# Performance work log

Measured on AMD Instinct MI355X. Metric: run time of the kernel, lower is better.

The kernel has to match this reference:

```python
import jax, jax.numpy as jnp
import numpy as np

EPS = 1e-7  # Keras backend epsilon


def setup_inputs() -> dict:
    key = jax.random.key(0)
    kx, ka, ke, kp = jax.random.split(key, 4)
    B, N, F, K_, C = 8, 2048, 128, 128, 128
    X = jax.random.normal(kx, (B, N, F), dtype=jnp.float32)
    Au = (jax.random.uniform(ka, (B, N, N)) < 0.05).astype(jnp.float32)
    A = jnp.maximum(Au, jnp.swapaxes(Au, -1, -2))
    W_emb = jax.random.normal(ke, (F, C), dtype=jnp.float32) * 0.1
    W_pool = jax.random.normal(kp, (F, K_), dtype=jnp.float32) * 0.1
    return {"X": X, "A": A, "W_emb": W_emb, "W_pool": W_pool}


def _diffpool(X, A, W_emb, W_pool):
    N = A.shape[-1]
    I = jnp.eye(N, dtype=A.dtype)
    A_ = A + I
    # symmetric normalization D^-1/2 (A+I) D^-1/2
    d = jax.lax.rsqrt(jnp.sum(A_, axis=-1))          # [B, N]
    fltr = A_ * d[..., :, None] * d[..., None, :]    # [B, N, N]

    Z = jnp.einsum('bnm,bmc->bnc', fltr, X @ W_emb)  # embedding GNN (no activation)
    S = jax.nn.softmax(jnp.einsum('bnm,bmk->bnk', fltr, X @ W_pool), axis=-1)  # [B, N, k]

    # link prediction loss: ||A - S S^T||_F per graph, mean over batch
    S_gram = jnp.einsum('bnk,bmk->bnm', S, S)
    LP_loss = jnp.mean(jnp.linalg.norm(A - S_gram, ord='fro', axis=(-1, -2)))

    # entropy loss on assignments
    entr = -jnp.sum(S * jnp.log(S + EPS), axis=-1)   # [B, N]
    entr_loss = jnp.mean(entr)

    X_pooled = jnp.einsum('bnk,bnc->bkc', S, Z)                  # S^T Z
    A_pooled = jnp.einsum('bnk,bnm,bml->bkl', S, A, S)           # S^T A S
    return X_pooled, A_pooled, S, LP_loss, entr_loss


def reference(X, A, W_emb, W_pool):
    return _diffpool(X, A, W_emb, W_pool)
```

## Files before the change

### kernel.cpp

```cpp
#include <hip/hip_runtime.h>
#include <math.h>

typedef __bf16 bf16x8 __attribute__((ext_vector_type(8)));
typedef float  f32x4  __attribute__((ext_vector_type(4)));
typedef unsigned short u16x4 __attribute__((ext_vector_type(4)));

#define DEVI __device__ __forceinline__

static constexpr int NB  = 8;
static constexpr int NN  = 2048;
static constexpr int NF  = 128;
static constexpr int NC2 = 256;
static constexpr int NSK = 16;

static constexpr int OUT_X0  = 0;
static constexpr int OUT_A0  = NB * 128 * 128;
static constexpr int OUT_S0  = OUT_A0 + NB * 128 * 128;
static constexpr int OUT_LP  = OUT_S0 + NB * NN * 128;
static constexpr int OUT_ENT = OUT_LP + 1;

DEVI unsigned short f2b(float f) {
  unsigned int u = __builtin_bit_cast(unsigned int, f);
  u += 0x7fffu + ((u >> 16) & 1u);
  return (unsigned short)(u >> 16);
}
DEVI float b2f(unsigned short h) {
  unsigned int u = ((unsigned int)h) << 16;
  return __builtin_bit_cast(float, u);
}
DEVI void load_lds16(const void* g, void* l) {
  __builtin_amdgcn_global_load_lds(
      (const __attribute__((address_space(1))) void*)g,
      (__attribute__((address_space(3))) void*)l, 16, 0, 0);
}
DEVI int swz(int row) { return (row >> 1) & 3; }

DEVI void stage_b128(const unsigned short* src, int ld, unsigned short* dst,
                     int k0, int tid) {
  const int wave = tid >> 6;
#pragma unroll
  for (int is = 0; is < 2; ++is) {
    const int row = is * 64 + (tid >> 2);
    const int c   = tid & 3;
    load_lds16(src + row * ld + k0 + ((c ^ swz(row)) << 3),
               dst + ((is * 256 + wave * 64) << 3));
  }
}
DEVI void stage_a64(const unsigned short* src, int ld, unsigned short* dst,
                    int k0, int tid) {
  const int wave = tid >> 6;
  const int row = tid >> 2, c = tid & 3;
  load_lds16(src + row * ld + k0 + ((c ^ swz(row)) << 3), dst + (wave << 9));
}

DEVI void gemm_core64(const unsigned short* Aop, int lda,
                      const unsigned short* Bop, int ldb, int ksteps,
                      unsigned short* lA0, unsigned short* lA1,
                      unsigned short* lB0, unsigned short* lB1,
                      int tid, f32x4 (&acc)[4][2]) {
  const int lane = tid & 63, wave = tid >> 6;
  const int l15 = lane & 15;
  const int sx = (lane >> 4) ^ ((l15 >> 1) & 3);
#pragma unroll
  for (int i = 0; i < 4; ++i) {
    acc[i][0] = (f32x4){0.f, 0.f, 0.f, 0.f};
    acc[i][1] = (f32x4){0.f, 0.f, 0.f, 0.f};
  }
  stage_a64(Aop, lda, lA0, 0, tid);
  stage_b128(Bop, ldb, lB0, 0, tid);
  __syncthreads();
  for (int kt = 0; kt < ksteps; ++kt) {
    unsigned short* curA = (kt & 1) ? lA1 : lA0;
    unsigned short* curB = (kt & 1) ? lB1 : lB0;
    if (kt + 1 < ksteps) {
      const int k0 = (kt + 1) * 32;
      stage_a64(Aop, lda, (kt & 1) ? lA0 : lA1, k0, tid);
      stage_b128(Bop, ldb, (kt & 1) ? lB0 : lB1, k0, tid);
    }
    bf16x8 af[4], bg[2];
#pragma unroll
    for (int i = 0; i < 4; ++i)
      af[i] = *(const bf16x8*)(curA + (((i * 16 + l15) * 4 + sx) << 3));
#pragma unroll
    for (int j = 0; j < 2; ++j)
      bg[j] = *(const bf16x8*)(curB + (((wave * 32 + j * 16 + l15) * 4 + sx) << 3));
#pragma unroll
    for (int i = 0; i < 4; ++i)
#pragma unroll
      for (int j = 0; j < 2; ++j)
        acc[i][j] = __builtin_amdgcn_mfma_f32_16x16x32_bf16(af[i], bg[j],
                                                            acc[i][j], 0, 0, 0);
    __syncthreads();
  }
}

DEVI void gemm_core128(const unsigned short* Aop, int lda,
                       const unsigned short* Bop, int ldb, int ksteps,
                       unsigned short* lA0, unsigned short* lA1,
                       unsigned short* lB0, unsigned short* lB1,
                       int tid, f32x4 (&acc)[4][4]) {
  const int lane = tid & 63, wave = tid >> 6;
  const int wr = wave >> 1, wc = wave & 1;
  const int l15 = lane & 15;
  const int sx = (lane >> 4) ^ ((l15 >> 1) & 3);
#pragma unroll
  for (int i = 0; i < 4; ++i)
#pragma unroll
    for (int j = 0; j < 4; ++j) acc[i][j] = (f32x4){0.f, 0.f, 0.f, 0.f};
  stage_b128(Aop, lda, lA0, 0, tid);
  stage_b128(Bop, ldb, lB0, 0, tid);
  __syncthreads();
  for (int kt = 0; kt < ksteps; ++kt) {
    unsigned short* curA = (kt & 1) ? lA1 : lA0;
    unsigned short* curB = (kt & 1) ? lB1 : lB0;
    if (kt + 1 < ksteps) {
      const int k0 = (kt + 1) * 32;
      stage_b128(Aop, lda, (kt & 1) ? lA0 : lA1, k0, tid);
      stage_b128(Bop, ldb, (kt & 1) ? lB0 : lB1, k0, tid);
    }
    bf16x8 af[4], bg[4];
#pragma unroll
    for (int i = 0; i < 4; ++i)
      af[i] = *(const bf16x8*)(curA + (((wr * 64 + i * 16 + l15) * 4 + sx) << 3));
#pragma unroll
    for (int j = 0; j < 4; ++j)
      bg[j] = *(const bf16x8*)(curB + (((wc * 64 + j * 16 + l15) * 4 + sx) << 3));
#pragma unroll
    for (int i = 0; i < 4; ++i)
#pragma unroll
      for (int j = 0; j < 4; ++j)
        acc[i][j] = __builtin_amdgcn_mfma_f32_16x16x32_bf16(af[i], bg[j],
                                                            acc[i][j], 0, 0, 0);
    __syncthreads();
  }
}

__global__ __launch_bounds__(256) void k_prep(const float* __restrict__ A,
                                              const float* __restrict__ X,
                                              const float* __restrict__ Wemb,
                                              const float* __restrict__ Wpool,
                                              unsigned short* __restrict__ AB,
                                              unsigned short* __restrict__ XB,
                                              unsigned short* __restrict__ WT,
                                              float* __restrict__ dvec,
                                              float* __restrict__ rsum) {
  const int blk = blockIdx.x, tid = threadIdx.x;
  if (blk < 4096) {
    const int row = blk * 4 + (tid >> 6);
    const int lane = tid & 63;
    const f32x4* src = (const f32x4*)(A + ((size_t)row << 11));
    u16x4* dst = (u16x4*)(AB + ((size_t)row << 11));
    float s = 0.f;
#pragma unroll
    for (int it = 0; it < 8; ++it) {
      f32x4 v = src[it * 64 + lane];
      s += v[0] + v[1] + v[2] + v[3];
      u16x4 o;
      o[0] = f2b(v[0]); o[1] = f2b(v[1]); o[2] = f2b(v[2]); o[3] = f2b(v[3]);
      dst[it * 64 + lane] = o;
    }
#pragma unroll
    for (int o2 = 32; o2; o2 >>= 1) s += __shfl_down(s, o2);
    if (lane == 0) { dvec[row] = rsqrtf(s + 1.f); rsum[row] = s; }
  } else if (blk < 4608) {
    const int i0 = (blk - 4096) * 1024 + tid;
    const f32x4* src = (const f32x4*)X;
    u16x4* dst = (u16x4*)XB;
#pragma unroll
    for (int it = 0; it < 4; ++it) {
      const int idx = i0 + it * 256;
      f32x4 v = src[idx];
      u16x4 o;
      o[0] = f2b(v[0]); o[1] = f2b(v[1]); o[2] = f2b(v[2]); o[3] = f2b(v[3]);
      dst[idx] = o;
    }
  } else {
    const int e = (blk - 4608) * 256 + tid;
    const int c = e >> 4, f0 = (e & 15) * 8;
    const float* W = (c < 128) ? Wemb : Wpool;
    const int cc = c & 127;
#pragma unroll
    for (int q = 0; q < 8; ++q)
      WT[c * 128 + f0 + q] = f2b(W[(f0 + q) * 128 + cc]);
  }
}

__global__ __launch_bounds__(256) void k_gemm_xw(const unsigned short* __restrict__ XB,
                                                 const unsigned short* __restrict__ WT,
                                                 const float* __restrict__ dvec,
                                                 unsigned short* __restrict__ VT) {
  __shared__ unsigned short lA[2][2048], lB[2][4096];
  const int mt = blockIdx.x, ct = blockIdx.y, tid = threadIdx.x;
  f32x4 acc[4][2];
  gemm_core64(XB + mt * 64 * NF, NF, WT + ct * 128 * NF, NF, NF / 32,
              lA[0], lA[1], lB[0], lB[1], tid, acc);
  const int lane = tid & 63, wave = tid >> 6;
  const int l15 = lane & 15, l4 = (lane >> 4) * 4;
#pragma unroll
  for (int i = 0; i < 4; ++i) {
    const int gr0 = mt * 64 + i * 16 + l4;
    const int b = gr0 >> 11, n0 = gr0 & 2047;
    const f32x4 dv = *(const f32x4*)(dvec + gr0);
#pragma unroll
    for (int j = 0; j < 2; ++j) {
      const int gc = ct * 128 + wave * 32 + j * 16 + l15;
      u16x4 pk;
#pragma unroll
      for (int r = 0; r < 4; ++r) pk[r] = f2b(acc[i][j][r] * dv[r]);
      *(u16x4*)(VT + (((size_t)(b * NC2 + gc)) << 11) + n0) = pk;
    }
  }
}

__global__ __launch_bounds__(256) void k_gemm_nv(const unsigned short* __restrict__ AB,
                                                 const unsigned short* __restrict__ VT,
                                                 const float* __restrict__ dvec,
                                                 unsigned short* __restrict__ YT,
                                                 float* __restrict__ out,
                                                 float* __restrict__ entv) {
  __shared__ unsigned short lA[2][2048], lB[2][4096];
  const int mt = blockIdx.x, ct = blockIdx.y, b = blockIdx.z, tid = threadIdx.x;
  const unsigned short* Aop = AB + ((size_t)b << 22) + (size_t)mt * 64 * NN;
  const unsigned short* Bop = VT + (((size_t)(b * NC2 + ct * 128)) << 11);
  f32x4 acc[4][2];
  gemm_core64(Aop, NN, Bop, NN, NN / 32, lA[0], lA[1], lB[0], lB[1], tid, acc);
  const int lane = tid & 63, wave = tid >> 6;
  const int l15 = lane & 15, l4g = lane >> 4, l4 = l4g * 4;
  f32x4 dv[4];
#pragma unroll
  for (int i = 0; i < 4; ++i)
    dv[i] = *(const f32x4*)(dvec + (b << 11) + mt * 64 + i * 16 + l4);
#pragma unroll
  for (int i = 0; i < 4; ++i) {
    const int n0 = mt * 64 + i * 16 + l4;
#pragma unroll
    for (int j = 0; j < 2; ++j) {
      const int c = ct * 128 + wave * 32 + j * 16 + l15;
      const u16x4 vv = *(const u16x4*)(VT + (((size_t)(b * NC2 + c)) << 11) + n0);
#pragma unroll
      for (int r = 0; r < 4; ++r)
        acc[i][j][r] = (acc[i][j][r] + b2f(vv[r])) * dv[i][r];
    }
  }
  if (ct == 0) {
#pragma unroll
    for (int i = 0; i < 4; ++i) {
      const int n0 = mt * 64 + i * 16 + l4;
#pragma unroll
      for (int j = 0; j < 2; ++j) {
        const int c = wave * 32 + j * 16 + l15;
        u16x4 pk;
#pragma unroll
        for (int r = 0; r < 4; ++r) pk[r] = f2b(acc[i][j][r]);
        *(u16x4*)(YT + (((size_t)(b * 384 + c)) << 11) + n0) = pk;
      }
    }
    return;
  }
  float* mbuf = (float*)lA;
  float* sbuf = mbuf + 256;
  float* tbuf = mbuf + 512;
  float* ebuf = mbuf + 768;
  float rm[4][4], rs[4][4], rt[4][4];
#pragma unroll
  for (int i = 0; i < 4; ++i)
#pragma unroll
    for (int r = 0; r < 4; ++r) {
      float m = fmaxf(acc[i][0][r], acc[i][1][r]);
#pragma unroll
      for (int off = 1; off < 16; off <<= 1) m = fmaxf(m, __shfl_xor(m, off));
      if (l15 == 0) mbuf[wave * 64 + i * 16 + l4 + r] = m;
    }
  __syncthreads();
#pragma unroll
  for (int i = 0; i < 4; ++i)
#pragma unroll
    for (int r = 0; r < 4; ++r) {
      const int row = i * 16 + l4 + r;
      rm[i][r] = fmaxf(fmaxf(mbuf[row], mbuf[64 + row]),
                       fmaxf(mbuf[128 + row], mbuf[192 + row]));
      rs[i][r] = 0.f; rt[i][r] = 0.f;
    }
#pragma unroll
  for (int i = 0; i < 4; ++i)
#pragma unroll
    for (int j = 0; j < 2; ++j)
#pragma unroll
      for (int r = 0; r < 4; ++r) {
        const float xm = acc[i][j][r] - rm[i][r];
        const float e = __expf(xm);
        acc[i][j][r] = e;
        rs[i][r] += e;
        rt[i][r] += xm * e;
      }
#pragma unroll
  for (int i = 0; i < 4; ++i)
#pragma unroll
    for (int r = 0; r < 4; ++r) {
      float s = rs[i][r], t = rt[i][r];
#pragma unroll
      for (int off = 1; off < 16; off <<= 1) {
        s += __shfl_xor(s, off); t += __shfl_xor(t, off);
      }
      if (l15 == 0) {
        sbuf[wave * 64 + i * 16 + l4 + r] = s;
        tbuf[wave * 64 + i * 16 + l4 + r] = t;
      }
    }
  __syncthreads();
  float ent = 0.f;
#pragma unroll
  for (int i = 0; i < 4; ++i)
#pragma unroll
    for (int r = 0; r < 4; ++r) {
      const int row = i * 16 + l4 + r;
      const float s = sbuf[row] + sbuf[64 + row] + sbuf[128 + row] + sbuf[192 + row];
      const float t = tbuf[row] + tbuf[64 + row] + tbuf[128 + row] + tbuf[192 + row];
      const float inv = 1.f / s;
      rs[i][r] = inv;
      ent += __logf(s) - t * inv;
    }
#pragma unroll
  for (int i = 0; i < 4; ++i) {
    const int n0 = mt * 64 + i * 16 + l4;
#pragma unroll
    for (int j = 0; j < 2; ++j) {
      const int c = wave * 32 + j * 16 + l15;
      u16x4 pk;
#pragma unroll
      for (int r = 0; r < 4; ++r) {
        const float sv = acc[i][j][r] * rs[i][r];
        pk[r] = f2b(sv);
        out[OUT_S0 + (((size_t)((b << 11) + n0 + r)) << 7) + c] = sv;
      }
      *(u16x4*)(YT + (((size_t)(b * 384 + 256 + c)) << 11) + n0) = pk;
    }
  }
  if (wave == 0 && l15 == 0) ebuf[l4g] = ent;
  __syncthreads();
  if (tid == 0)
    entv[b * 32 + mt] = ebuf[0] + ebuf[1] + ebuf[2] + ebuf[3];
}

__global__ __launch_bounds__(256) void k_gemm_as(const unsigned short* __restrict__ AB,
                                                 unsigned short* __restrict__ YT) {
  __shared__ unsigned short lA[2][2048], lB[2][4096];
  const int mt = blockIdx.x, b = blockIdx.z, tid = threadIdx.x;
  const unsigned short* Aop = AB + ((size_t)b << 22) + (size_t)mt * 64 * NN;
  const unsigned short* Bop = YT + (((size_t)(b * 384 + 256)) << 11);
  f32x4 acc[4][2];
  gemm_core64(Aop, NN, Bop, NN, NN / 32, lA[0], lA[1], lB[0], lB[1], tid, acc);
  const int lane = tid & 63, wave = tid >> 6;
  const int l15 = lane & 15, l4 = (lane >> 4) * 4;
#pragma unroll
  for (int i = 0; i < 4; ++i) {
    const int n0 = mt * 64 + i * 16 + l4;
#pragma unroll
    for (int j = 0; j < 2; ++j) {
      const int c = wave * 32 + j * 16 + l15;
      u16x4 pk;
#pragma unroll
      for (int r = 0; r < 4; ++r) pk[r] = f2b(acc[i][j][r]);
      *(u16x4*)(YT + (((size_t)(b * 384 + 128 + c)) << 11) + n0) = pk;
    }
  }
}

__global__ __launch_bounds__(256) void k_gemm_p(const unsigned short* __restrict__ YT,
                                                float* __restrict__ Pp) {
  __shared__ unsigned short lA[2][4096], lB[2][4096];
  const int ct = blockIdx.x, sk = blockIdx.y, b = blockIdx.z, tid = threadIdx.x;
  const unsigned short* Aop = YT + (((size_t)(b * 384 + 256)) << 11) + sk * 128;
  const unsigned short* Bop = YT + (((size_t)(b * 384 + ct * 128)) << 11) + sk * 128;
  f32x4 acc[4][4];
  gemm_core128(Aop, NN, Bop, NN, 4, lA[0], lA[1], lB[0], lB[1], tid, acc);
  const int lane = tid & 63, wave = tid >> 6;
  const int wr = wave >> 1, wc = wave & 1, l15 = lane & 15, l4 = (lane >> 4) * 4;
  float* dst = Pp + ((size_t)(sk * NB + b)) * 128 * 384;
#pragma unroll
  for (int i = 0; i < 4; ++i) {
    const int p0 = wr * 64 + i * 16 + l4;
#pragma unroll
    for (int j = 0; j < 4; ++j) {
      const int gc = ct * 128 + wc * 64 + j * 16 + l15;
#pragma unroll
      for (int r = 0; r < 4; ++r) dst[(p0 + r) * 384 + gc] = acc[i][j][r];
    }
  }
}

__global__ __launch_bounds__(256) void k_reduce_p(const float* __restrict__ Pp,
                                                  float* __restrict__ trp,
                                                  float* __restrict__ g2p,
                                                  float* __restrict__ out) {
  const int chunk = blockIdx.x, b = blockIdx.y, tid = threadIdx.x;
  const int e = chunk * 256 + tid;
  const int p = e / 384, c = e - p * 384;
  float s = 0.f;
#pragma unroll
  for (int sk = 0; sk < NSK; ++sk)
    s += Pp[((size_t)(sk * NB + b)) * (128 * 384) + e];
  float tr = 0.f, g2 = 0.f;
  if (c < 128) {
    out[OUT_X0 + ((size_t)(b * 128 + p)) * 128 + c] = s;
  } else if (c < 256) {
    out[OUT_A0 + ((size_t)(b * 128 + p)) * 128 + (c - 128)] = s;
    if (c - 128 == p) tr = s;
  } else {
    g2 = s * s;
  }
  __shared__ float rb[512];
  rb[tid] = tr; rb[256 + tid] = g2;
  __syncthreads();
  for (int o = 128; o; o >>= 1) {
    if (tid < o) { rb[tid] += rb[tid + o]; rb[256 + tid] += rb[256 + tid + o]; }
    __syncthreads();
  }
  if (tid == 0) { trp[b * 192 + chunk] = rb[0]; g2p[b * 192 + chunk] = rb[256]; }
}

__global__ __launch_bounds__(256) void k_lp(const float* __restrict__ rsum,
                                            const float* __restrict__ trp,
                                            const float* __restrict__ g2p,
                                            float* __restrict__ lpv) {
  const int b = blockIdx.x, tid = threadIdx.x;
  float nz = 0.f;
#pragma unroll
  for (int i = 0; i < 8; ++i) nz += rsum[(b << 11) + i * 256 + tid];
  float tr = (tid < 192) ? trp[b * 192 + tid] : 0.f;
  float g2 = (tid < 192) ? g2p[b * 192 + tid] : 0.f;
  __shared__ float rb[768];
  rb[tid] = nz; rb[256 + tid] = tr; rb[512 + tid] = g2;
  __syncthreads();
  for (int o = 128; o; o >>= 1) {
    if (tid < o) {
      rb[tid] += rb[tid + o];
      rb[256 + tid] += rb[256 + tid + o];
      rb[512 + tid] += rb[512 + tid + o];
    }
    __syncthreads();
  }
  if (tid == 0)
    lpv[b] = sqrtf(fmaxf(rb[0] - 2.f * rb[256] + rb[512], 0.f));
}

__global__ __launch_bounds__(256) void k_losses(const float* __restrict__ entv,
                                                const float* __restrict__ lpv,
                                                float* __restrict__ out) {
  const int tid = threadIdx.x;
  __shared__ float rb[256];
  rb[tid] = entv[tid];
  __syncthreads();
  for (int o = 128; o; o >>= 1) {
    if (tid < o) rb[tid] += rb[tid + o];
    __syncthreads();
  }
  if (tid == 0) {
    float lp = 0.f;
#pragma unroll
    for (int b = 0; b < 8; ++b) lp += lpv[b];
    out[OUT_LP] = 0.125f * lp;
    out[OUT_ENT] = rb[0] * (1.f / (NB * NN));
  }
}

extern "C" void kernel_launch(void* const* d_in, const int* in_sizes, int n_in,
                              void* d_out, int out_size, void* d_ws, size_t ws_size,
                              hipStream_t stream) {
  const float* X     = (const float*)d_in[0];
  const float* A     = (const float*)d_in[1];
  const float* Wemb  = (const float*)d_in[2];
  const float* Wpool = (const float*)d_in[3];
  float* out = (float*)d_out;

  char* ws = (char*)d_ws;
  size_t o = 0;
  unsigned short* AB = (unsigned short*)(ws + o); o += (size_t)NB * NN * NN * 2;
  unsigned short* XB = (unsigned short*)(ws + o); o += (size_t)NB * NN * NF * 2;
  unsigned short* WT = (unsigned short*)(ws + o); o += (size_t)NC2 * NF * 2;
  unsigned short* VT = (unsigned short*)(ws + o); o += (size_t)NB * NC2 * NN * 2;
  unsigned short* YT = (unsigned short*)(ws + o); o += (size_t)NB * 384 * NN * 2;
  float* Pp  = (float*)(ws + o); o += (size_t)NSK * NB * 128 * 384 * 4;
  float* dvec = (float*)(ws + o); o += (size_t)NB * NN * 4;
  float* rsum = (float*)(ws + o); o += (size_t)NB * NN * 4;
  float* trp  = (float*)(ws + o); o += (size_t)NB * 192 * 4;
  float* g2p  = (float*)(ws + o); o += (size_t)NB * 192 * 4;
  float* entv = (float*)(ws + o); o += 256 * 4;
  float* lpv  = (float*)(ws + o); o += NB * 4;

  k_prep    <<<dim3(4624), 256, 0, stream>>>(A, X, Wemb, Wpool, AB, XB, WT, dvec, rsum);
  k_gemm_xw <<<dim3(NB * NN / 64, 2), 256, 0, stream>>>(XB, WT, dvec, VT);
  k_gemm_nv <<<dim3(NN / 64, 2, NB), 256, 0, stream>>>(AB, VT, dvec, YT, out, entv);
  k_gemm_as <<<dim3(NN / 64, 1, NB), 256, 0, stream>>>(AB, YT);
  k_gemm_p  <<<dim3(3, NSK, NB), 256, 0, stream>>>(YT, Pp);
  k_reduce_p<<<dim3(192, NB), 256, 0, stream>>>(Pp, trp, g2p, out);
  k_lp      <<<dim3(NB), 256, 0, stream>>>(rsum, trp, g2p, lpv);
  k_losses  <<<1, 256, 0, stream>>>(entv, lpv, out);
}
```

Measured before the change: 308.7 us.

## Fuse four GEMM stages into one persistent kernel with grid barriers

Replaces the four separate GEMM launches (XW, normalized A·V with softmax, A·S, and the pooled products) with a single 512-block kernel. A software grid barrier built on atomic counters separates the stages, and a small zeroing kernel resets the counters before each run. The goal is to remove launch gaps and tail effects between dependent stages. In exchange, it requires all 512 blocks to be co-resident, hence launch_bounds(256,2) and shared LDS. It also adds barrier spin cost, and later stages leave many blocks idle (256 or 384 of 512 active).

```diff
diff --git a/kernel.cpp b/kernel.cpp
--- a/kernel.cpp
+++ b/kernel.cpp
@@ -12,6 +12,7 @@
 static constexpr int NF  = 128;
 static constexpr int NC2 = 256;
 static constexpr int NSK = 16;
+static constexpr int NG  = 512;
 
 static constexpr int OUT_X0  = 0;
 static constexpr int OUT_A0  = NB * 128 * 128;
@@ -19,6 +20,9 @@
 static constexpr int OUT_LP  = OUT_S0 + NB * NN * 128;
 static constexpr int OUT_ENT = OUT_LP + 1;
 
+static constexpr int BAR_STRIDE = 65 * 32;
+static constexpr int BAR_UINTS  = 3 * BAR_STRIDE;
+
 DEVI unsigned short f2b(float f) {
   unsigned int u = __builtin_bit_cast(unsigned int, f);
   u += 0x7fffu + ((u >> 16) & 1u);
@@ -35,29 +39,44 @@
 }
 DEVI int swz(int row) { return (row >> 1) & 3; }
 
-DEVI void stage_b128(const unsigned short* src, int ld, unsigned short* dst,
-                     int k0, int tid) {
-  const int wave = tid >> 6;
-#pragma unroll
-  for (int is = 0; is < 2; ++is) {
-    const int row = is * 64 + (tid >> 2);
-    const int c   = tid & 3;
-    load_lds16(src + row * ld + k0 + ((c ^ swz(row)) << 3),
-               dst + ((is * 256 + wave * 64) << 3));
-  }
-}
+DEVI void gbar(unsigned* bar, int phase, int tid, int bid) {
+  __syncthreads();
+  if (tid == 0) {
+    __threadfence();
+    unsigned* base = bar + phase * BAR_STRIDE;
+    if (atomicAdd(base + ((bid >> 3) << 5), 1u) == 7u)
+      atomicAdd(base + 2048, 1u);
+    while (__hip_atomic_load(base + 2048, __ATOMIC_RELAXED,
+                             __HIP_MEMORY_SCOPE_AGENT) < 64u)
+      __builtin_amdgcn_s_sleep(2);
+    __threadfence();
+  }
+  __syncthreads();
+}
+
 DEVI void stage_a64(const unsigned short* src, int ld, unsigned short* dst,
                     int k0, int tid) {
   const int wave = tid >> 6;
   const int row = tid >> 2, c = tid & 3;
-  load_lds16(src + row * ld + k0 + ((c ^ swz(row)) << 3), dst + (wave << 9));
-}
-
-DEVI void gemm_core64(const unsigned short* Aop, int lda,
-                      const unsigned short* Bop, int ldb, int ksteps,
-                      unsigned short* lA0, unsigned short* lA1,
-                      unsigned short* lB0, unsigned short* lB1,
-                      int tid, f32x4 (&acc)[4][2]) {
+  load_lds16(src + (size_t)row * ld + k0 + ((c ^ swz(row)) << 3), dst + (wave << 9));
+}
+DEVI void stage_b128(const unsigned short* src, int ld, unsigned short* dst,
+                     int k0, int tid) {
+  const int wave = tid >> 6;
+#pragma unroll
+  for (int is = 0; is < 2; ++is) {
+    const int row = is * 64 + (tid >> 2);
+    const int c   = tid & 3;
+    load_lds16(src + (size_t)row * ld + k0 + ((c ^ swz(row)) << 3),
+               dst + ((is * 256 + wave * 64) << 3));
+  }
+}
+
+DEVI void core64(const unsigned short* Aop, int lda,
+                 const unsigned short* Bop, int ldb, int ksteps,
+                 unsigned short* lA0, unsigned short* lA1,
+                 unsigned short* lB0, unsigned short* lB1,
+                 int tid, f32x4 (&acc)[4][2]) {
   const int lane = tid & 63, wave = tid >> 6;
   const int l15 = lane & 15;
   const int sx = (lane >> 4) ^ ((l15 >> 1) & 3);
@@ -94,11 +113,11 @@
   }
 }
 
-DEVI void gemm_core128(const unsigned short* Aop, int lda,
-                       const unsigned short* Bop, int ldb, int ksteps,
-                       unsigned short* lA0, unsigned short* lA1,
-                       unsigned short* lB0, unsigned short* lB1,
-                       int tid, f32x4 (&acc)[4][4]) {
+DEVI void core128(const unsigned short* Aop, int lda,
+                  const unsigned short* Bop, int ldb, int ksteps,
+                  unsigned short* lA0, unsigned short* lA1,
+                  unsigned short* lB0, unsigned short* lB1,
+                  int tid, f32x4 (&acc)[4][4]) {
   const int lane = tid & 63, wave = tid >> 6;
   const int wr = wave >> 1, wc = wave & 1;
   const int l15 = lane & 15;
@@ -133,6 +152,11 @@
                                                             acc[i][j], 0, 0, 0);
     __syncthreads();
   }
+}
+
+__global__ __launch_bounds__(256) void k_zero(unsigned* __restrict__ bar) {
+  const int idx = blockIdx.x * 256 + threadIdx.x;
+  if (idx < BAR_UINTS) bar[idx] = 0u;
 }
 
 __global__ __launch_bounds__(256) void k_prep(const float* __restrict__ A,
@@ -168,11 +192,10 @@
     u16x4* dst = (u16x4*)XB;
 #pragma unroll
     for (int it = 0; it < 4; ++it) {
-      const int idx = i0 + it * 256;
-      f32x4 v = src[idx];
+      f32x4 v = src[i0 + it * 256];
       u16x4 o;
       o[0] = f2b(v[0]); o[1] = f2b(v[1]); o[2] = f2b(v[2]); o[3] = f2b(v[3]);
-      dst[idx] = o;
+      dst[i0 + it * 256] = o;
     }
   } else {
     const int e = (blk - 4608) * 256 + tid;
@@ -185,64 +208,171 @@
   }
 }
 
-__global__ __launch_bounds__(256) void k_gemm_xw(const unsigned short* __restrict__ XB,
-                                                 const unsigned short* __restrict__ WT,
-                                                 const float* __restrict__ dvec,
-                                                 unsigned short* __restrict__ VT) {
-  __shared__ unsigned short lA[2][2048], lB[2][4096];
-  const int mt = blockIdx.x, ct = blockIdx.y, tid = threadIdx.x;
-  f32x4 acc[4][2];
-  gemm_core64(XB + mt * 64 * NF, NF, WT + ct * 128 * NF, NF, NF / 32,
-              lA[0], lA[1], lB[0], lB[1], tid, acc);
-  const int lane = tid & 63, wave = tid >> 6;
-  const int l15 = lane & 15, l4 = (lane >> 4) * 4;
-#pragma unroll
-  for (int i = 0; i < 4; ++i) {
-    const int gr0 = mt * 64 + i * 16 + l4;
-    const int b = gr0 >> 11, n0 = gr0 & 2047;
-    const f32x4 dv = *(const f32x4*)(dvec + gr0);
-#pragma unroll
-    for (int j = 0; j < 2; ++j) {
-      const int gc = ct * 128 + wave * 32 + j * 16 + l15;
-      u16x4 pk;
-#pragma unroll
-      for (int r = 0; r < 4; ++r) pk[r] = f2b(acc[i][j][r] * dv[r]);
-      *(u16x4*)(VT + (((size_t)(b * NC2 + gc)) << 11) + n0) = pk;
-    }
-  }
-}
-
-__global__ __launch_bounds__(256) void k_gemm_nv(const unsigned short* __restrict__ AB,
-                                                 const unsigned short* __restrict__ VT,
-                                                 const float* __restrict__ dvec,
-                                                 unsigned short* __restrict__ YT,
-                                                 float* __restrict__ out,
-                                                 float* __restrict__ entv) {
-  __shared__ unsigned short lA[2][2048], lB[2][4096];
-  const int mt = blockIdx.x, ct = blockIdx.y, b = blockIdx.z, tid = threadIdx.x;
-  const unsigned short* Aop = AB + ((size_t)b << 22) + (size_t)mt * 64 * NN;
-  const unsigned short* Bop = VT + (((size_t)(b * NC2 + ct * 128)) << 11);
-  f32x4 acc[4][2];
-  gemm_core64(Aop, NN, Bop, NN, NN / 32, lA[0], lA[1], lB[0], lB[1], tid, acc);
+__global__ __launch_bounds__(256, 2) void k_gemms(
+    const unsigned short* __restrict__ XB, const unsigned short* __restrict__ WT,
+    unsigned short* __restrict__ AB, unsigned short* __restrict__ VT,
+    unsigned short* __restrict__ YT, const float* __restrict__ dvec,
+    float* __restrict__ out, float* __restrict__ entv,
+    float* __restrict__ Pp, unsigned* __restrict__ bar) {
+  __shared__ __align__(16) unsigned char smem[40960];
+  unsigned short* sm16 = (unsigned short*)smem;
+  float* smf = (float*)smem;
+  const int bid = blockIdx.x, tid = threadIdx.x;
   const int lane = tid & 63, wave = tid >> 6;
   const int l15 = lane & 15, l4g = lane >> 4, l4 = l4g * 4;
-  f32x4 dv[4];
-#pragma unroll
-  for (int i = 0; i < 4; ++i)
-    dv[i] = *(const f32x4*)(dvec + (b << 11) + mt * 64 + i * 16 + l4);
-#pragma unroll
-  for (int i = 0; i < 4; ++i) {
-    const int n0 = mt * 64 + i * 16 + l4;
-#pragma unroll
-    for (int j = 0; j < 2; ++j) {
-      const int c = ct * 128 + wave * 32 + j * 16 + l15;
-      const u16x4 vv = *(const u16x4*)(VT + (((size_t)(b * NC2 + c)) << 11) + n0);
-#pragma unroll
-      for (int r = 0; r < 4; ++r)
-        acc[i][j][r] = (acc[i][j][r] + b2f(vv[r])) * dv[i][r];
-    }
-  }
-  if (ct == 0) {
+
+  {
+    const int mt = bid >> 1, ct = bid & 1;
+    f32x4 acc[4][2];
+    core64(XB + mt * 64 * NF, NF, WT + ct * 128 * NF, NF, NF / 32,
+           sm16, sm16 + 2048, sm16 + 4096, sm16 + 8192, tid, acc);
+#pragma unroll
+    for (int i = 0; i < 4; ++i) {
+      const int gr0 = mt * 64 + i * 16 + l4;
+      const int b = gr0 >> 11, n0 = gr0 & 2047;
+      const f32x4 dv = *(const f32x4*)(dvec + gr0);
+#pragma unroll
+      for (int j = 0; j < 2; ++j) {
+        const int gc = ct * 128 + wave * 32 + j * 16 + l15;
+        u16x4 pk;
+#pragma unroll
+        for (int r = 0; r < 4; ++r) pk[r] = f2b(acc[i][j][r] * dv[r]);
+        *(u16x4*)(VT + (((size_t)(b * NC2 + gc)) << 11) + n0) = pk;
+      }
+    }
+  }
+  gbar(bar, 0, tid, bid);
+
+  {
+    const int mt = bid & 31, b = (bid >> 5) & 7, ct = bid >> 8;
+    const unsigned short* Aop = AB + ((size_t)b << 22) + (size_t)mt * 64 * NN;
+    const unsigned short* Bop = VT + (((size_t)(b * NC2 + ct * 128)) << 11);
+    f32x4 acc[4][2];
+    core64(Aop, NN, Bop, NN, NN / 32, sm16, sm16 + 2048, sm16 + 4096, sm16 + 8192,
+           tid, acc);
+    f32x4 dv[4];
+#pragma unroll
+    for (int i = 0; i < 4; ++i)
+      dv[i] = *(const f32x4*)(dvec + (b << 11) + mt * 64 + i * 16 + l4);
+#pragma unroll
+    for (int i = 0; i < 4; ++i) {
+      const int n0 = mt * 64 + i * 16 + l4;
+#pragma unroll
+      for (int j = 0; j < 2; ++j) {
+        const int c = ct * 128 + wave * 32 + j * 16 + l15;
+        const u16x4 vv = *(const u16x4*)(VT + (((size_t)(b * NC2 + c)) << 11) + n0);
+#pragma unroll
+        for (int r = 0; r < 4; ++r)
+          acc[i][j][r] = (acc[i][j][r] + b2f(vv[r])) * dv[i][r];
+      }
+    }
+    if (ct == 0) {
+#pragma unroll
+      for (int i = 0; i < 4; ++i) {
+        const int n0 = mt * 64 + i * 16 + l4;
+#pragma unroll
+        for (int j = 0; j < 2; ++j) {
+          const int c = wave * 32 + j * 16 + l15;
+          u16x4 pk;
+#pragma unroll
+          for (int r = 0; r < 4; ++r) pk[r] = f2b(acc[i][j][r]);
+          *(u16x4*)(YT + (((size_t)(b * 384 + c)) << 11) + n0) = pk;
+        }
+      }
+    } else {
+      float* mbuf = smf;
+      float* sbuf = smf + 256;
+      float* tbuf = smf + 512;
+      float* ebuf = smf + 768;
+      float rm[4][4], rs[4][4], rt[4][4];
+#pragma unroll
+      for (int i = 0; i < 4; ++i)
+#pragma unroll
+        for (int r = 0; r < 4; ++r) {
+          float m = fmaxf(acc[i][0][r], acc[i][1][r]);
+#pragma unroll
+          for (int off = 1; off < 16; off <<= 1) m = fmaxf(m, __shfl_xor(m, off));
+          if (l15 == 0) mbuf[wave * 64 + i * 16 + l4 + r] = m;
+        }
+      __syncthreads();
+#pragma unroll
+      for (int i = 0; i < 4; ++i)
+#pragma unroll
+        for (int r = 0; r < 4; ++r) {
+          const int row = i * 16 + l4 + r;
+          rm[i][r] = fmaxf(fmaxf(mbuf[row], mbuf[64 + row]),
+                           fmaxf(mbuf[128 + row], mbuf[192 + row]));
+          rs[i][r] = 0.f; rt[i][r] = 0.f;
+        }
+#pragma unroll
+      for (int i = 0; i < 4; ++i)
+#pragma unroll
+        for (int j = 0; j < 2; ++j)
+#pragma unroll
+          for (int r = 0; r < 4; ++r) {
+            const float xm = acc[i][j][r] - rm[i][r];
+            const float e = __expf(xm);
+            acc[i][j][r] = e;
+            rs[i][r] += e;
+            rt[i][r] += xm * e;
+          }
+#pragma unroll
+      for (int i = 0; i < 4; ++i)
+#pragma unroll
+        for (int r = 0; r < 4; ++r) {
+          float s = rs[i][r], t = rt[i][r];
+#pragma unroll
+          for (int off = 1; off < 16; off <<= 1) {
+            s += __shfl_xor(s, off); t += __shfl_xor(t, off);
+          }
+          if (l15 == 0) {
+            sbuf[wave * 64 + i * 16 + l4 + r] = s;
+            tbuf[wave * 64 + i * 16 + l4 + r] = t;
+          }
+        }
+      __syncthreads();
+      float ent = 0.f;
+#pragma unroll
+      for (int i = 0; i < 4; ++i)
+#pragma unroll
+        for (int r = 0; r < 4; ++r) {
+          const int row = i * 16 + l4 + r;
+          const float s = sbuf[row] + sbuf[64+row] + sbuf[128+row] + sbuf[192+row];
+          const float t = tbuf[row] + tbuf[64+row] + tbuf[128+row] + tbuf[192+row];
+          const float inv = 1.f / s;
+          rs[i][r] = inv;
+          ent += __logf(s) - t * inv;
+        }
+#pragma unroll
+      for (int i = 0; i < 4; ++i) {
+        const int n0 = mt * 64 + i * 16 + l4;
+#pragma unroll
+        for (int j = 0; j < 2; ++j) {
+          const int c = wave * 32 + j * 16 + l15;
+          u16x4 pk;
+#pragma unroll
+          for (int r = 0; r < 4; ++r) {
+            const float sv = acc[i][j][r] * rs[i][r];
+            pk[r] = f2b(sv);
+            out[OUT_S0 + (((size_t)((b << 11) + n0 + r)) << 7) + c] = sv;
+          }
+          *(u16x4*)(YT + (((size_t)(b * 384 + 256 + c)) << 11) + n0) = pk;
+        }
+      }
+      if (wave == 0 && l15 == 0) ebuf[l4g] = ent;
+      __syncthreads();
+      if (tid == 0)
+        entv[b * 32 + mt] = ebuf[0] + ebuf[1] + ebuf[2] + ebuf[3];
+    }
+  }
+  gbar(bar, 1, tid, bid);
+
+  if (bid < 256) {
+    const int mt = bid & 31, b = bid >> 5;
+    f32x4 acc[4][2];
+    core64(AB + ((size_t)b << 22) + (size_t)mt * 64 * NN, NN,
+           YT + (((size_t)(b * 384 + 256)) << 11), NN, NN / 32,
+           sm16, sm16 + 2048, sm16 + 4096, sm16 + 8192, tid, acc);
 #pragma unroll
     for (int i = 0; i < 4; ++i) {
       const int n0 = mt * 64 + i * 16 + l4;
@@ -252,139 +382,30 @@
         u16x4 pk;
 #pragma unroll
         for (int r = 0; r < 4; ++r) pk[r] = f2b(acc[i][j][r]);
-        *(u16x4*)(YT + (((size_t)(b * 384 + c)) << 11) + n0) = pk;
+        *(u16x4*)(YT + (((size_t)(b * 384 + 128 + c)) << 11) + n0) = pk;
       }
     }
-    return;
-  }
-  float* mbuf = (float*)lA;
-  float* sbuf = mbuf + 256;
-  float* tbuf = mbuf + 512;
-  float* ebuf = mbuf + 768;
-  float rm[4][4], rs[4][4], rt[4][4];
-#pragma unroll
-  for (int i = 0; i < 4; ++i)
-#pragma unroll
-    for (int r = 0; r < 4; ++r) {
-      float m = fmaxf(acc[i][0][r], acc[i][1][r]);
-#pragma unroll
-      for (int off = 1; off < 16; off <<= 1) m = fmaxf(m, __shfl_xor(m, off));
-      if (l15 == 0) mbuf[wave * 64 + i * 16 + l4 + r] = m;
-    }
-  __syncthreads();
-#pragma unroll
-  for (int i = 0; i < 4; ++i)
-#pragma unroll
-    for (int r = 0; r < 4; ++r) {
-      const int row = i * 16 + l4 + r;
-      rm[i][r] = fmaxf(fmaxf(mbuf[row], mbuf[64 + row]),
-                       fmaxf(mbuf[128 + row], mbuf[192 + row]));
-      rs[i][r] = 0.f; rt[i][r] = 0.f;
-    }
-#pragma unroll
-  for (int i = 0; i < 4; ++i)
-#pragma unroll
-    for (int j = 0; j < 2; ++j)
-#pragma unroll
-      for (int r = 0; r < 4; ++r) {
-        const float xm = acc[i][j][r] - rm[i][r];
-        const float e = __expf(xm);
-        acc[i][j][r] = e;
-        rs[i][r] += e;
-        rt[i][r] += xm * e;
+  }
+  gbar(bar, 2, tid, bid);
+
+  if (bid < 384) {
+    const int ct = bid % 3, u = bid / 3;
+    const int sk = u & 15, b = u >> 4;
+    f32x4 acc[4][4];
+    core128(YT + (((size_t)(b * 384 + 256)) << 11) + sk * 128, NN,
+            YT + (((size_t)(b * 384 + ct * 128)) << 11) + sk * 128, NN, 4,
+            sm16, sm16 + 4096, sm16 + 8192, sm16 + 12288, tid, acc);
+    const int wr = wave >> 1, wc = wave & 1;
+    float* dst = Pp + ((size_t)(sk * NB + b)) * 128 * 384;
+#pragma unroll
+    for (int i = 0; i < 4; ++i) {
+      const int p0 = wr * 64 + i * 16 + l4;
+#pragma unroll
+      for (int j = 0; j < 4; ++j) {
+        const int gc = ct * 128 + wc * 64 + j * 16 + l15;
+#pragma unroll
+        for (int r = 0; r < 4; ++r) dst[(p0 + r) * 384 + gc] = acc[i][j][r];
       }
-#pragma unroll
-  for (int i = 0; i < 4; ++i)
-#pragma unroll
-    for (int r = 0; r < 4; ++r) {
-      float s = rs[i][r], t = rt[i][r];
-#pragma unroll
-      for (int off = 1; off < 16; off <<= 1) {
-        s += __shfl_xor(s, off); t += __shfl_xor(t, off);
-      }
-      if (l15 == 0) {
-        sbuf[wave * 64 + i * 16 + l4 + r] = s;
-        tbuf[wave * 64 + i * 16 + l4 + r] = t;
-      }
-    }
-  __syncthreads();
-  float ent = 0.f;
-#pragma unroll
-  for (int i = 0; i < 4; ++i)
-#pragma unroll
-    for (int r = 0; r < 4; ++r) {
-      const int row = i * 16 + l4 + r;
-      const float s = sbuf[row] + sbuf[64 + row] + sbuf[128 + row] + sbuf[192 + row];
-      const float t = tbuf[row] + tbuf[64 + row] + tbuf[128 + row] + tbuf[192 + row];
-      const float inv = 1.f / s;
-      rs[i][r] = inv;
-      ent += __logf(s) - t * inv;
-    }
-#pragma unroll
-  for (int i = 0; i < 4; ++i) {
-    const int n0 = mt * 64 + i * 16 + l4;
-#pragma unroll
-    for (int j = 0; j < 2; ++j) {
-      const int c = wave * 32 + j * 16 + l15;
-      u16x4 pk;
-#pragma unroll
-      for (int r = 0; r < 4; ++r) {
-        const float sv = acc[i][j][r] * rs[i][r];
-        pk[r] = f2b(sv);
-        out[OUT_S0 + (((size_t)((b << 11) + n0 + r)) << 7) + c] = sv;
-      }
-      *(u16x4*)(YT + (((size_t)(b * 384 + 256 + c)) << 11) + n0) = pk;
-    }
-  }
-  if (wave == 0 && l15 == 0) ebuf[l4g] = ent;
-  __syncthreads();
-  if (tid == 0)
-    entv[b * 32 + mt] = ebuf[0] + ebuf[1] + ebuf[2] + ebuf[3];
-}
-
-__global__ __launch_bounds__(256) void k_gemm_as(const unsigned short* __restrict__ AB,
-                                                 unsigned short* __restrict__ YT) {
-  __shared__ unsigned short lA[2][2048], lB[2][4096];
-  const int mt = blockIdx.x, b = blockIdx.z, tid = threadIdx.x;
-  const unsigned short* Aop = AB + ((size_t)b << 22) + (size_t)mt * 64 * NN;
-  const unsigned short* Bop = YT + (((size_t)(b * 384 + 256)) << 11);
-  f32x4 acc[4][2];
-  gemm_core64(Aop, NN, Bop, NN, NN / 32, lA[0], lA[1], lB[0], lB[1], tid, acc);
-  const int lane = tid & 63, wave = tid >> 6;
-  const int l15 = lane & 15, l4 = (lane >> 4) * 4;
-#pragma unroll
-  for (int i = 0; i < 4; ++i) {
-    const int n0 = mt * 64 + i * 16 + l4;
-#pragma unroll
-    for (int j = 0; j < 2; ++j) {
-      const int c = wave * 32 + j * 16 + l15;
-      u16x4 pk;
-#pragma unroll
-      for (int r = 0; r < 4; ++r) pk[r] = f2b(acc[i][j][r]);
-      *(u16x4*)(YT + (((size_t)(b * 384 + 128 + c)) << 11) + n0) = pk;
-    }
-  }
-}
-
-__global__ __launch_bounds__(256) void k_gemm_p(const unsigned short* __restrict__ YT,
-                                                float* __restrict__ Pp) {
-  __shared__ unsigned short lA[2][4096], lB[2][4096];
-  const int ct = blockIdx.x, sk = blockIdx.y, b = blockIdx.z, tid = threadIdx.x;
-  const unsigned short* Aop = YT + (((size_t)(b * 384 + 256)) << 11) + sk * 128;
-  const unsigned short* Bop = YT + (((size_t)(b * 384 + ct * 128)) << 11) + sk * 128;
-  f32x4 acc[4][4];
-  gemm_core128(Aop, NN, Bop, NN, 4, lA[0], lA[1], lB[0], lB[1], tid, acc);
-  const int lane = tid & 63, wave = tid >> 6;
-  const int wr = wave >> 1, wc = wave & 1, l15 = lane & 15, l4 = (lane >> 4) * 4;
-  float* dst = Pp + ((size_t)(sk * NB + b)) * 128 * 384;
-#pragma unroll
-  for (int i = 0; i < 4; ++i) {
-    const int p0 = wr * 64 + i * 16 + l4;
-#pragma unroll
-    for (int j = 0; j < 4; ++j) {
-      const int gc = ct * 128 + wc * 64 + j * 16 + l15;
-#pragma unroll
-      for (int r = 0; r < 4; ++r) dst[(p0 + r) * 384 + gc] = acc[i][j][r];
     }
   }
 }
@@ -487,12 +508,11 @@
   float* g2p  = (float*)(ws + o); o += (size_t)NB * 192 * 4;
   float* entv = (float*)(ws + o); o += 256 * 4;
   float* lpv  = (float*)(ws + o); o += NB * 4;
-
+  unsigned* bar = (unsigned*)(ws + o); o += BAR_UINTS * 4;
+
+  k_zero    <<<dim3((BAR_UINTS + 255) / 256), 256, 0, stream>>>(bar);
   k_prep    <<<dim3(4624), 256, 0, stream>>>(A, X, Wemb, Wpool, AB, XB, WT, dvec, rsum);
-  k_gemm_xw <<<dim3(NB * NN / 64, 2), 256, 0, stream>>>(XB, WT, dvec, VT);
-  k_gemm_nv <<<dim3(NN / 64, 2, NB), 256, 0, stream>>>(AB, VT, dvec, YT, out, entv);
-  k_gemm_as <<<dim3(NN / 64, 1, NB), 256, 0, stream>>>(AB, YT);
-  k_gemm_p  <<<dim3(3, NSK, NB), 256, 0, stream>>>(YT, Pp);
+  k_gemms   <<<dim3(NG), 256, 0, stream>>>(XB, WT, AB, VT, YT, dvec, out, entv, Pp, bar);
   k_reduce_p<<<dim3(192, NB), 256, 0, stream>>>(Pp, trp, g2p, out);
   k_lp      <<<dim3(NB), 256, 0, stream>>>(rsum, trp, g2p, lpv);
   k_losses  <<<1, 256, 0, stream>>>(entv, lpv, out);
```

Result: slower. 395.1 us (+28.0%).

## Deepen 64-row GEMM pipeline to four LDS stages with explicit vmcnt waits

Applied to the files above, without the earlier changes.

Replaces the double-buffered 64x128 GEMM core with a 4-slot ring that keeps three k-tiles of global-to-LDS loads in flight. It waits with graded s_waitcnt vmcnt values and raw s_barrier instead of __syncthreads. The aim is to hide global memory latency in the long-K adjacency GEMMs (2048 deep). In exchange, LDS use per block doubles to 48KB, which may reduce occupancy, and the hand-written waitcnt counts assume exactly three loads per stage.

```diff
diff --git a/kernel.cpp b/kernel.cpp
--- a/kernel.cpp
+++ b/kernel.cpp
@@ -35,29 +35,28 @@
 }
 DEVI int swz(int row) { return (row >> 1) & 3; }
 
-DEVI void stage_b128(const unsigned short* src, int ld, unsigned short* dst,
-                     int k0, int tid) {
-  const int wave = tid >> 6;
-#pragma unroll
-  for (int is = 0; is < 2; ++is) {
-    const int row = is * 64 + (tid >> 2);
-    const int c   = tid & 3;
-    load_lds16(src + row * ld + k0 + ((c ^ swz(row)) << 3),
-               dst + ((is * 256 + wave * 64) << 3));
-  }
-}
 DEVI void stage_a64(const unsigned short* src, int ld, unsigned short* dst,
                     int k0, int tid) {
   const int wave = tid >> 6;
   const int row = tid >> 2, c = tid & 3;
-  load_lds16(src + row * ld + k0 + ((c ^ swz(row)) << 3), dst + (wave << 9));
-}
-
-DEVI void gemm_core64(const unsigned short* Aop, int lda,
-                      const unsigned short* Bop, int ldb, int ksteps,
-                      unsigned short* lA0, unsigned short* lA1,
-                      unsigned short* lB0, unsigned short* lB1,
-                      int tid, f32x4 (&acc)[4][2]) {
+  load_lds16(src + (size_t)row * ld + k0 + ((c ^ swz(row)) << 3), dst + (wave << 9));
+}
+DEVI void stage_b128(const unsigned short* src, int ld, unsigned short* dst,
+                     int k0, int tid) {
+  const int wave = tid >> 6;
+#pragma unroll
+  for (int is = 0; is < 2; ++is) {
+    const int row = is * 64 + (tid >> 2);
+    const int c   = tid & 3;
+    load_lds16(src + (size_t)row * ld + k0 + ((c ^ swz(row)) << 3),
+               dst + ((is * 256 + wave * 64) << 3));
+  }
+}
+
+DEVI void core64p(const unsigned short* Aop, int lda,
+                  const unsigned short* Bop, int ldb, int ksteps,
+                  unsigned short* lA, unsigned short* lB,
+                  int tid, f32x4 (&acc)[4][2]) {
   const int lane = tid & 63, wave = tid >> 6;
   const int l15 = lane & 15;
   const int sx = (lane >> 4) ^ ((l15 >> 1) & 3);
@@ -66,17 +65,28 @@
     acc[i][0] = (f32x4){0.f, 0.f, 0.f, 0.f};
     acc[i][1] = (f32x4){0.f, 0.f, 0.f, 0.f};
   }
-  stage_a64(Aop, lda, lA0, 0, tid);
-  stage_b128(Bop, ldb, lB0, 0, tid);
-  __syncthreads();
+#pragma unroll
+  for (int t = 0; t < 3; ++t) {
+    if (t < ksteps) {
+      stage_a64(Aop, lda, lA + t * 2048, t * 32, tid);
+      stage_b128(Bop, ldb, lB + t * 4096, t * 32, tid);
+    }
+  }
+#pragma unroll 1
   for (int kt = 0; kt < ksteps; ++kt) {
-    unsigned short* curA = (kt & 1) ? lA1 : lA0;
-    unsigned short* curB = (kt & 1) ? lB1 : lB0;
-    if (kt + 1 < ksteps) {
-      const int k0 = (kt + 1) * 32;
-      stage_a64(Aop, lda, (kt & 1) ? lA0 : lA1, k0, tid);
-      stage_b128(Bop, ldb, (kt & 1) ? lB0 : lB1, k0, tid);
-    }
+    const int cur = kt & 3;
+    if (kt + 3 < ksteps) {
+      stage_a64(Aop, lda, lA + ((kt + 3) & 3) * 2048, (kt + 3) * 32, tid);
+      stage_b128(Bop, ldb, lB + ((kt + 3) & 3) * 4096, (kt + 3) * 32, tid);
+    }
+    const int rem = ksteps - 1 - kt;
+    if (rem >= 3)      asm volatile("s_waitcnt vmcnt(9)" ::: "memory");
+    else if (rem == 2) asm volatile("s_waitcnt vmcnt(6)" ::: "memory");
+    else if (rem == 1) asm volatile("s_waitcnt vmcnt(3)" ::: "memory");
+    else               asm volatile("s_waitcnt vmcnt(0)" ::: "memory");
+    __builtin_amdgcn_s_barrier();
+    const unsigned short* curA = lA + cur * 2048;
+    const unsigned short* curB = lB + cur * 4096;
     bf16x8 af[4], bg[2];
 #pragma unroll
     for (int i = 0; i < 4; ++i)
@@ -90,15 +100,16 @@
       for (int j = 0; j < 2; ++j)
         acc[i][j] = __builtin_amdgcn_mfma_f32_16x16x32_bf16(af[i], bg[j],
                                                             acc[i][j], 0, 0, 0);
-    __syncthreads();
-  }
-}
-
-DEVI void gemm_core128(const unsigned short* Aop, int lda,
-                       const unsigned short* Bop, int ldb, int ksteps,
-                       unsigned short* lA0, unsigned short* lA1,
-                       unsigned short* lB0, unsigned short* lB1,
-                       int tid, f32x4 (&acc)[4][4]) {
+    asm volatile("s_waitcnt lgkmcnt(0)" ::: "memory");
+    __builtin_amdgcn_s_barrier();
+  }
+}
+
+DEVI void core128(const unsigned short* Aop, int lda,
+                  const unsigned short* Bop, int ldb, int ksteps,
+                  unsigned short* lA0, unsigned short* lA1,
+                  unsigned short* lB0, unsigned short* lB1,
+                  int tid, f32x4 (&acc)[4][4]) {
   const int lane = tid & 63, wave = tid >> 6;
   const int wr = wave >> 1, wc = wave & 1;
   const int l15 = lane & 15;
@@ -168,11 +179,10 @@
     u16x4* dst = (u16x4*)XB;
 #pragma unroll
     for (int it = 0; it < 4; ++it) {
-      const int idx = i0 + it * 256;
-      f32x4 v = src[idx];
+      f32x4 v = src[i0 + it * 256];
       u16x4 o;
       o[0] = f2b(v[0]); o[1] = f2b(v[1]); o[2] = f2b(v[2]); o[3] = f2b(v[3]);
-      dst[idx] = o;
+      dst[i0 + it * 256] = o;
     }
   } else {
     const int e = (blk - 4608) * 256 + tid;
@@ -189,11 +199,10 @@
                                                  const unsigned short* __restrict__ WT,
                                                  const float* __restrict__ dvec,
                                                  unsigned short* __restrict__ VT) {
-  __shared__ unsigned short lA[2][2048], lB[2][4096];
+  __shared__ __align__(16) unsigned short lA[4 * 2048], lB[4 * 4096];
   const int mt = blockIdx.x, ct = blockIdx.y, tid = threadIdx.x;
   f32x4 acc[4][2];
-  gemm_core64(XB + mt * 64 * NF, NF, WT + ct * 128 * NF, NF, NF / 32,
-              lA[0], lA[1], lB[0], lB[1], tid, acc);
+  core64p(XB + mt * 64 * NF, NF, WT + ct * 128 * NF, NF, NF / 32, lA, lB, tid, acc);
   const int lane = tid & 63, wave = tid >> 6;
   const int l15 = lane & 15, l4 = (lane >> 4) * 4;
 #pragma unroll
@@ -218,12 +227,12 @@
                                                  unsigned short* __restrict__ YT,
                                                  float* __restrict__ out,
                                                  float* __restrict__ entv) {
-  __shared__ unsigned short lA[2][2048], lB[2][4096];
+  __shared__ __align__(16) unsigned short lA[4 * 2048], lB[4 * 4096];
   const int mt = blockIdx.x, ct = blockIdx.y, b = blockIdx.z, tid = threadIdx.x;
   const unsigned short* Aop = AB + ((size_t)b << 22) + (size_t)mt * 64 * NN;
   const unsigned short* Bop = VT + (((size_t)(b * NC2 + ct * 128)) << 11);
   f32x4 acc[4][2];
-  gemm_core64(Aop, NN, Bop, NN, NN / 32, lA[0], lA[1], lB[0], lB[1], tid, acc);
+  core64p(Aop, NN, Bop, NN, NN / 32, lA, lB, tid, acc);
   const int lane = tid & 63, wave = tid >> 6;
   const int l15 = lane & 15, l4g = lane >> 4, l4 = l4g * 4;
   f32x4 dv[4];
@@ -344,12 +353,11 @@
 
 __global__ __launch_bounds__(256) void k_gemm_as(const unsigned short* __restrict__ AB,
                                                  unsigned short* __restrict__ YT) {
-  __shared__ unsigned short lA[2][2048], lB[2][4096];
+  __shared__ __align__(16) unsigned short lA[4 * 2048], lB[4 * 4096];
   const int mt = blockIdx.x, b = blockIdx.z, tid = threadIdx.x;
-  const unsigned short* Aop = AB + ((size_t)b << 22) + (size_t)mt * 64 * NN;
-  const unsigned short* Bop = YT + (((size_t)(b * 384 + 256)) << 11);
   f32x4 acc[4][2];
-  gemm_core64(Aop, NN, Bop, NN, NN / 32, lA[0], lA[1], lB[0], lB[1], tid, acc);
+  core64p(AB + ((size_t)b << 22) + (size_t)mt * 64 * NN, NN,
+          YT + (((size_t)(b * 384 + 256)) << 11), NN, NN / 32, lA, lB, tid, acc);
   const int lane = tid & 63, wave = tid >> 6;
   const int l15 = lane & 15, l4 = (lane >> 4) * 4;
 #pragma unroll
@@ -368,12 +376,12 @@
 
 __global__ __launch_bounds__(256) void k_gemm_p(const unsigned short* __restrict__ YT,
                                                 float* __restrict__ Pp) {
-  __shared__ unsigned short lA[2][4096], lB[2][4096];
+  __shared__ __align__(16) unsigned short lA[2][4096], lB[2][4096];
   const int ct = blockIdx.x, sk = blockIdx.y, b = blockIdx.z, tid = threadIdx.x;
-  const unsigned short* Aop = YT + (((size_t)(b * 384 + 256)) << 11) + sk * 128;
-  const unsigned short* Bop = YT + (((size_t)(b * 384 + ct * 128)) << 11) + sk * 128;
   f32x4 acc[4][4];
-  gemm_core128(Aop, NN, Bop, NN, 4, lA[0], lA[1], lB[0], lB[1], tid, acc);
+  core128(YT + (((size_t)(b * 384 + 256)) << 11) + sk * 128, NN,
+          YT + (((size_t)(b * 384 + ct * 128)) << 11) + sk * 128, NN, 4,
+          lA[0], lA[1], lB[0], lB[1], tid, acc);
   const int lane = tid & 63, wave = tid >> 6;
   const int wr = wave >> 1, wc = wave & 1, l15 = lane & 15, l4 = (lane >> 4) * 4;
   float* dst = Pp + ((size_t)(sk * NB + b)) * 128 * 384;
```

Measured after the change: 322.0 us. 4.3% more time.
